# Performance work log

Measured on AMD Instinct MI355X. Metric: run time of the kernel, lower is better.

The kernel has to match this reference:

```python
import jax, jax.numpy as jnp
import numpy as np

N = 50000
E = 1600000
EPS = 1e-5


def setup_inputs() -> dict:
    key = jax.random.key(0)
    ks = jax.random.split(key, 10)
    x = jax.random.normal(ks[0], (N, 128), dtype=jnp.float32)
    edge_row = jax.random.randint(ks[1], (E,), 0, N, dtype=jnp.int32)
    edge_col = jax.random.randint(ks[2], (E,), 0, N, dtype=jnp.int32)
    edge_weight = jax.random.uniform(ks[3], (E,), dtype=jnp.float32)
    # kaiming-ish scaled weights
    W0 = jax.random.normal(ks[4], (128, 128), dtype=jnp.float32) / np.sqrt(128)
    b0 = jax.random.normal(ks[5], (128,), dtype=jnp.float32) * 0.01
    W1 = jax.random.normal(ks[6], (128, 128), dtype=jnp.float32) / np.sqrt(128)
    b1 = jax.random.normal(ks[7], (128,), dtype=jnp.float32) * 0.01
    W2 = jax.random.normal(ks[8], (128, 40), dtype=jnp.float32) / np.sqrt(128)
    b2 = jax.random.normal(ks[9], (40,), dtype=jnp.float32) * 0.01
    g0 = jnp.ones((128,), jnp.float32)
    be0 = jnp.zeros((128,), jnp.float32)
    g1 = jnp.ones((128,), jnp.float32)
    be1 = jnp.zeros((128,), jnp.float32)
    return dict(x=x, edge_row=edge_row, edge_col=edge_col, edge_weight=edge_weight,
                W0=W0, b0=b0, g0=g0, be0=be0, W1=W1, b1=b1, g1=g1, be1=be1, W2=W2, b2=b2)


def _spmm(edge_row, edge_col, edge_weight, h):
    # adj_t @ h : gather source rows, scale by edge weight, scatter-add to dst
    msg = h[edge_col] * edge_weight[:, None]           # [E, F]
    return jax.ops.segment_sum(msg, edge_row, num_segments=N)  # [N, F]


def _gcn_conv(x, W, b, edge_row, edge_col, edge_weight):
    h = x @ W                                          # dense GEMM [N, F_out]
    return _spmm(edge_row, edge_col, edge_weight, h) + b


def _batchnorm(x, gamma, beta):
    # training-mode BatchNorm1d over node dim (biased variance, as torch uses)
    mean = jnp.mean(x, axis=0)
    var = jnp.mean(jnp.square(x - mean), axis=0)
    return (x - mean) * jax.lax.rsqrt(var + EPS) * gamma + beta


def reference(x, edge_row, edge_col, edge_weight,
              W0, b0, g0, be0, W1, b1, g1, be1, W2, b2):
    # layer 0: conv -> BN -> ReLU (dropout = identity for deterministic reference)
    h = _gcn_conv(x, W0, b0, edge_row, edge_col, edge_weight)
    h = jax.nn.relu(_batchnorm(h, g0, be0))
    # layer 1
    h = _gcn_conv(h, W1, b1, edge_row, edge_col, edge_weight)
    h = jax.nn.relu(_batchnorm(h, g1, be1))
    # final conv (no BN/ReLU)
    return _gcn_conv(h, W2, b2, edge_row, edge_col, edge_weight)
```

## Files before the change

### kernel.cpp

```cpp
#include <hip/hip_runtime.h>
#include <hip/hip_fp16.h>


constexpr int   N_NODES   = 50000;
constexpr int   E_EDGES   = 1600000;
constexpr float BN_EPS    = 1e-5f;
constexpr int   K_BUCKETS = (N_NODES + 255) / 256;
constexpr int   BCAP      = 10240;
constexpr int   CHUNK     = 4096;
constexpr int   PART_BLK  = (E_EDGES + CHUNK - 1) / CHUNK;
constexpr int   CG_SHIFT  = 13;
constexpr int   CG_N      = 8;
constexpr int   AITER     = CHUNK / 256;
constexpr int   TEAMS40   = 6;

typedef _Float16 f16x8 __attribute__((ext_vector_type(8)));
typedef float    f32x4 __attribute__((ext_vector_type(4)));
typedef float    f32x2 __attribute__((ext_vector_type(2)));

__device__ __forceinline__ float dec_w(unsigned u) {
  return __half2float(__ushort_as_half((unsigned short)(u >> 16)));
}

__global__ __launch_bounds__(128) void prep_ker(const float* __restrict__ W0,
                                                const float* __restrict__ W1,
                                                const float* __restrict__ W2,
                                                __half* __restrict__ wt0,
                                                __half* __restrict__ wt1,
                                                __half* __restrict__ wt2,
                                                float* __restrict__ zstats) {
  const int b = blockIdx.x;
  const int k = threadIdx.x;
  if (b == 0) {
#pragma unroll
    for (int j = 0; j < 6; ++j) zstats[k * 6 + j] = 0.f;
  }
  if (b < 128) {
    wt0[b * 128 + k] = __float2half_rn(W0[k * 128 + b]);
  } else if (b < 256) {
    const int n = b - 128;
    wt1[n * 128 + k] = __float2half_rn(W1[k * 128 + n]);
  } else {
    const int n = b - 256;
    const float v = (n < 40) ? W2[k * 40 + n] : 0.f;
    wt2[n * 128 + k] = __float2half_rn(v);
  }
}

__global__ __launch_bounds__(256) void partA_ker(const int* __restrict__ rows,
                                                 const int* __restrict__ cols,
                                                 const float* __restrict__ ew,
                                                 int* __restrict__ gcursor,
                                                 int2* __restrict__ ebuf) {
  __shared__ int  cnt[256], cnt2[256], sc[256], offs[256], gbase[256];
  __shared__ int2 buf[CHUNK];
  const int tid = threadIdx.x;
  cnt[tid] = 0; cnt2[tid] = 0;
  __syncthreads();

  const int e0   = blockIdx.x * CHUNK;
  const int ecnt = min(CHUNK, E_EDGES - e0);

  int2 held[AITER];
#pragma unroll
  for (int j = 0; j < AITER; ++j) {
    const int i = tid + j * 256;
    if (i < ecnt) {
      const int   r = rows[e0 + i];
      const int   c = cols[e0 + i];
      const float w = ew[e0 + i];
      held[j].x = c | ((int)__half_as_ushort(__float2half_rn(w)) << 16);
      held[j].y = r;
      atomicAdd(&cnt[r >> 8], 1);
    }
  }
  __syncthreads();

  sc[tid] = cnt[tid];
  __syncthreads();
  for (int o = 1; o < 256; o <<= 1) {
    int u = (tid >= o) ? sc[tid - o] : 0;
    __syncthreads();
    sc[tid] += u;
    __syncthreads();
  }
  offs[tid] = sc[tid] - cnt[tid];
  if (tid < K_BUCKETS && cnt[tid] > 0)
    gbase[tid] = atomicAdd(&gcursor[tid], cnt[tid]);
  __syncthreads();

#pragma unroll
  for (int j = 0; j < AITER; ++j) {
    const int i = tid + j * 256;
    if (i < ecnt) {
      const int b = held[j].y >> 8;
      const int p = offs[b] + atomicAdd(&cnt2[b], 1);
      buf[p] = held[j];
    }
  }
  __syncthreads();

  for (int i = tid; i < ecnt; i += 256) {
    const int2 v   = buf[i];
    const int  b   = v.y >> 8;
    const int  idx = gbase[b] + (i - offs[b]);
    if (idx < BCAP) ebuf[(long)b * BCAP + idx] = v;
  }
}

__global__ __launch_bounds__(256) void partB_ker(const int* __restrict__ gcursor,
                                                 const int2* __restrict__ ebuf,
                                                 unsigned* __restrict__ se,
                                                 int* __restrict__ rowptr) {
  const int b   = blockIdx.x;
  const int tid = threadIdx.x;
  __shared__ int cnt[256 * CG_N], cur[256 * CG_N], sh[256];
  __shared__ int sbase;

  const int gv = (tid < K_BUCKETS) ? gcursor[tid] : 0;
  sh[tid] = gv;
  __syncthreads();
  for (int o = 1; o < 256; o <<= 1) {
    int u = (tid >= o) ? sh[tid - o] : 0;
    __syncthreads();
    sh[tid] += u;
    __syncthreads();
  }
  if (tid == b) sbase = sh[tid] - gv;
  if (b == 0 && tid == 0) rowptr[N_NODES] = E_EDGES;

#pragma unroll
  for (int j = 0; j < CG_N; ++j) {
    cnt[tid * CG_N + j] = 0;
    cur[tid * CG_N + j] = 0;
  }
  __syncthreads();
  const int base = sbase;
  const int cntb = min(gcursor[b], BCAP);

  const int2* __restrict__ src = ebuf + (long)b * BCAP;
  for (int i = tid; i < cntb; i += 256) {
    const int2 v = src[i];
    const int key = (v.y & 255) * CG_N + ((v.x & 0xFFFF) >> CG_SHIFT);
    atomicAdd(&cnt[key], 1);
  }
  __syncthreads();

  int loc[CG_N];
  int s = 0;
#pragma unroll
  for (int j = 0; j < CG_N; ++j) { loc[j] = s; s += cnt[tid * CG_N + j]; }
  sh[tid] = s;
  __syncthreads();
  for (int o = 1; o < 256; o <<= 1) {
    int u = (tid >= o) ? sh[tid - o] : 0;
    __syncthreads();
    sh[tid] += u;
    __syncthreads();
  }
  const int tb = sh[tid] - s;
#pragma unroll
  for (int j = 0; j < CG_N; ++j) cnt[tid * CG_N + j] = tb + loc[j];
  const int grow = b * 256 + tid;
  if (grow < N_NODES) rowptr[grow] = base + tb;
  __syncthreads();

  for (int i = tid; i < cntb; i += 256) {
    const int2 v   = src[i];
    const int  key = (v.y & 255) * CG_N + ((v.x & 0xFFFF) >> CG_SHIFT);
    const int  p   = cnt[key] + atomicAdd(&cur[key], 1);
    se[base + p] = (unsigned)v.x;
  }
}

template <int FOUT, int FOUT_PAD, bool FUSE, bool OUT_FP8, typename XT>
__global__ __launch_bounds__(256) void gemm_mfma_ker(const XT* __restrict__ X,
                                                     const __half* __restrict__ Wt,
                                                     void* __restrict__ Hout,
                                                     const float* __restrict__ stats,
                                                     const float* __restrict__ g,
                                                     const float* __restrict__ be) {
  constexpr int CT    = FOUT_PAD / 16;
  constexpr int PITCH = 136;

  __shared__ _Float16 Xs[64 * PITCH];
  __shared__ _Float16 Ws[FOUT_PAD * PITCH];
  __shared__ float ssc[128], ssh[128];

  const int tid  = threadIdx.x;
  const int row0 = blockIdx.x * 64;

  if constexpr (FUSE) {
    if (tid < 128) {
      const float mean = stats[tid] * (1.0f / N_NODES);
      const float var  = stats[128 + tid] * (1.0f / N_NODES) - mean * mean;
      const float sc   = g[tid] * rsqrtf(var + BN_EPS);
      ssc[tid] = sc;
      ssh[tid] = be[tid] - mean * sc;
    }
    __syncthreads();
  }

  for (int i = tid; i < FOUT_PAD * 16; i += 256) {
    const int r  = i >> 4;
    const int c8 = (i & 15) * 8;
    *(f16x8*)(Ws + r * PITCH + c8) = *(const f16x8*)(Wt + r * 128 + c8);
  }

  if constexpr (sizeof(XT) == 4) {
    for (int i = tid; i < 64 * 32; i += 256) {
      const int r  = i >> 5;
      const int k4 = (i & 31) * 4;
      const int gr = min(row0 + r, N_NODES - 1);
      float4 v = *(const float4*)((const float*)X + (long)gr * 128 + k4);
      _Float16* d = Xs + r * PITCH + k4;
      d[0] = (_Float16)v.x; d[1] = (_Float16)v.y;
      d[2] = (_Float16)v.z; d[3] = (_Float16)v.w;
    }
  } else {
    for (int i = tid; i < 64 * 16; i += 256) {
      const int r  = i >> 4;
      const int k8 = (i & 15) * 8;
      const int gr = min(row0 + r, N_NODES - 1);
      f16x8 v = *(const f16x8*)((const _Float16*)X + (long)gr * 128 + k8);
      if constexpr (FUSE) {
#pragma unroll
        for (int j = 0; j < 8; ++j)
          v[j] = (_Float16)fmaxf((float)v[j] * ssc[k8 + j] + ssh[k8 + j], 0.f);
      }
      *(f16x8*)(Xs + r * PITCH + k8) = v;
    }
  }
  __syncthreads();

  const int wave = tid >> 6;
  const int lane = tid & 63;
  const int m    = lane & 15;
  const int q    = lane >> 4;
  const int rw   = wave * 16;

  f16x8 af[4];
  {
    const _Float16* ab = Xs + (rw + m) * PITCH + q * 8;
#pragma unroll
    for (int ks = 0; ks < 4; ++ks) af[ks] = *(const f16x8*)(ab + ks * 32);
  }

  f32x4 acc[CT];
#pragma unroll
  for (int ct = 0; ct < CT; ++ct) acc[ct] = (f32x4){0.f, 0.f, 0.f, 0.f};

#pragma unroll
  for (int ct = 0; ct < CT; ++ct) {
    const _Float16* bb = Ws + (ct * 16 + m) * PITCH + q * 8;
#pragma unroll
    for (int ks = 0; ks < 4; ++ks) {
      const f16x8 bf = *(const f16x8*)(bb + ks * 32);
      acc[ct] = __builtin_amdgcn_mfma_f32_16x16x32_f16(af[ks], bf, acc[ct], 0, 0, 0);
    }
  }

  __syncthreads();
#pragma unroll
  for (int ct = 0; ct < CT; ++ct) {
#pragma unroll
    for (int reg = 0; reg < 4; ++reg) {
      Xs[(rw + q * 4 + reg) * PITCH + ct * 16 + m] = (_Float16)acc[ct][reg];
    }
  }
  __syncthreads();

  if constexpr (OUT_FP8) {
    constexpr int C16 = FOUT / 16;
    unsigned char* H8 = (unsigned char*)Hout;
    for (int i = tid; i < 64 * C16; i += 256) {
      const int r   = i / C16;
      const int c16 = (i % C16) * 16;
      const int gr  = row0 + r;
      if (gr < N_NODES) {
        const _Float16* src = Xs + r * PITCH + c16;
        int w[4];
#pragma unroll
        for (int j = 0; j < 4; ++j) {
          int p = __builtin_amdgcn_cvt_pk_fp8_f32((float)src[4 * j + 0],
                                                  (float)src[4 * j + 1], 0, false);
          p = __builtin_amdgcn_cvt_pk_fp8_f32((float)src[4 * j + 2],
                                              (float)src[4 * j + 3], p, true);
          w[j] = p;
        }
        *(int4*)(H8 + (long)gr * FOUT + c16) = make_int4(w[0], w[1], w[2], w[3]);
      }
    }
  } else {
    constexpr int C8 = FOUT / 8;
    __half* H16 = (__half*)Hout;
    for (int i = tid; i < 64 * C8; i += 256) {
      const int r  = i / C8;
      const int c8 = (i % C8) * 8;
      const int gr = row0 + r;
      if (gr < N_NODES)
        *(f16x8*)(H16 + (long)gr * FOUT + c8) = *(const f16x8*)(Xs + r * PITCH + c8);
    }
  }
}

__global__ __launch_bounds__(256) void spmm_fp8_ker(const int* __restrict__ rowptr,
                                                    const unsigned* __restrict__ se,
                                                    const unsigned char* __restrict__ H,
                                                    __half* __restrict__ A) {
  const int gid  = blockIdx.x * 256 + threadIdx.x;
  const int lane = threadIdx.x & 63;
  const int wid  = __builtin_amdgcn_readfirstlane(gid >> 6);
  if (wid >= N_NODES) return;
  const int beg = rowptr[wid];
  const int end = rowptr[wid + 1];
  const ushort* __restrict__ Hl = (const ushort*)H + lane;
  float acc0 = 0.f, acc1 = 0.f;

#define FP8_EDGE(U)                                                            \
  {                                                                            \
    const unsigned u_ = (U);                                                   \
    const f32x2 v_ = __builtin_amdgcn_cvt_pk_f32_fp8((int)Hl[(u_ & 0xFFFF) * 64], false); \
    const float w_ = dec_w(u_);                                                \
    acc0 += w_ * v_[0]; acc1 += w_ * v_[1];                                    \
  }

  int e = beg;
  for (; e < end && (e & 3); ++e) FP8_EDGE(se[e]);
  for (; e + 8 <= end; e += 8) {
    const uint4 a = *(const uint4*)(se + e);
    const uint4 b = *(const uint4*)(se + e + 4);
    FP8_EDGE(a.x) FP8_EDGE(a.y) FP8_EDGE(a.z) FP8_EDGE(a.w)
    FP8_EDGE(b.x) FP8_EDGE(b.y) FP8_EDGE(b.z) FP8_EDGE(b.w)
  }
  for (; e + 4 <= end; e += 4) {
    const uint4 a = *(const uint4*)(se + e);
    FP8_EDGE(a.x) FP8_EDGE(a.y) FP8_EDGE(a.z) FP8_EDGE(a.w)
  }
  for (; e < end; ++e) FP8_EDGE(se[e]);
#undef FP8_EDGE

  ((__half2*)A)[(long)wid * 64 + lane] = __floats2half2_rn(acc0, acc1);
}

__global__ __launch_bounds__(256) void spmm_csr40_ker(const int* __restrict__ rowptr,
                                                      const unsigned* __restrict__ se,
                                                      const __half* __restrict__ H,
                                                      const float* __restrict__ b,
                                                      float* __restrict__ out) {
  const int t    = threadIdx.x;
  const int team = t / 40;
  const int l    = t % 40;
  if (team >= TEAMS40) return;
  const int wid = blockIdx.x * TEAMS40 + team;
  if (wid >= N_NODES) return;
  const int beg = rowptr[wid];
  const int end = rowptr[wid + 1];
  float acc = 0.f;

#define F40_EDGE(U)                                                            \
  {                                                                            \
    const unsigned u_ = (U);                                                   \
    acc += dec_w(u_) * __half2float(H[(long)(u_ & 0xFFFF) * 40 + l]);          \
  }

  int e = beg;
  for (; e < end && (e & 3); ++e) F40_EDGE(se[e]);
  for (; e + 8 <= end; e += 8) {
    const uint4 a = *(const uint4*)(se + e);
    const uint4 c = *(const uint4*)(se + e + 4);
    F40_EDGE(a.x) F40_EDGE(a.y) F40_EDGE(a.z) F40_EDGE(a.w)
    F40_EDGE(c.x) F40_EDGE(c.y) F40_EDGE(c.z) F40_EDGE(c.w)
  }
  for (; e + 4 <= end; e += 4) {
    const uint4 a = *(const uint4*)(se + e);
    F40_EDGE(a.x) F40_EDGE(a.y) F40_EDGE(a.z) F40_EDGE(a.w)
  }
  for (; e < end; ++e) F40_EDGE(se[e]);
#undef F40_EDGE

  __builtin_nontemporal_store(acc + b[l], out + (long)wid * 40 + l);
}

constexpr int BN_BLOCKS   = 512;
constexpr int BN_ROWS_PER = (N_NODES + BN_BLOCKS - 1) / BN_BLOCKS;

__global__ __launch_bounds__(256) void bn_stats_ker(const __half* __restrict__ A,
                                                    float* __restrict__ stats) {
  __shared__ float s_sh[128], q_sh[128];
  const int tid = threadIdx.x;
  if (tid < 128) { s_sh[tid] = 0.f; q_sh[tid] = 0.f; }
  __syncthreads();

  const int c2 = (tid & 63) * 2;
  const int rs = tid >> 6;
  const int r0 = blockIdx.x * BN_ROWS_PER;
  const int re = min(r0 + BN_ROWS_PER, N_NODES);
  float s0 = 0.f, s1 = 0.f, q0 = 0.f, q1 = 0.f;
  for (int r = r0 + rs; r < re; r += 4) {
    const float2 v = __half22float2(*(const __half2*)(A + (long)r * 128 + c2));
    s0 += v.x; q0 += v.x * v.x;
    s1 += v.y; q1 += v.y * v.y;
  }
  atomicAdd(&s_sh[c2 + 0], s0);
  atomicAdd(&s_sh[c2 + 1], s1);
  atomicAdd(&q_sh[c2 + 0], q0);
  atomicAdd(&q_sh[c2 + 1], q1);
  __syncthreads();
  if (tid < 128) {
    atomicAdd(&stats[tid],       s_sh[tid]);
    atomicAdd(&stats[128 + tid], q_sh[tid]);
  }
}

extern "C" void kernel_launch(void* const* d_in, const int* in_sizes, int n_in,
                              void* d_out, int out_size, void* d_ws, size_t ws_size,
                              hipStream_t stream) {
  const float* x    = (const float*)d_in[0];
  const int*   erow = (const int*)d_in[1];
  const int*   ecol = (const int*)d_in[2];
  const float* ew   = (const float*)d_in[3];
  const float* W0   = (const float*)d_in[4];
  const float* g0   = (const float*)d_in[6];
  const float* be0  = (const float*)d_in[7];
  const float* W1   = (const float*)d_in[8];
  const float* g1   = (const float*)d_in[10];
  const float* be1  = (const float*)d_in[11];
  const float* W2   = (const float*)d_in[12];
  const float* b2   = (const float*)d_in[13];
  float* out = (float*)d_out;

  unsigned char* h  = (unsigned char*)d_ws;
  __half*   agg     = (__half*)(h + (long)N_NODES * 256);
  float*    stats0  = (float*)(agg + (long)N_NODES * 128);
  float*    stats1  = stats0 + 256;
  int*      gcursor = (int*)(stats1 + 256);
  int*      rowptr  = gcursor + 256;
  unsigned* se      = (unsigned*)(rowptr + 50004);
  int2*     ebuf    = (int2*)(se + E_EDGES);
  __half*   wt0     = (__half*)(ebuf + (long)K_BUCKETS * BCAP);
  __half*   wt1     = wt0 + 128 * 128;
  __half*   wt2     = wt1 + 128 * 128;

  const int g_gemm   = (N_NODES + 63) / 64;
  const int g_spmm   = (N_NODES * 64) / 256;
  const int g_spmm40 = (N_NODES + TEAMS40 - 1) / TEAMS40;

  prep_ker<<<304, 128, 0, stream>>>(W0, W1, W2, wt0, wt1, wt2, stats0);

  partA_ker<<<PART_BLK, 256, 0, stream>>>(erow, ecol, ew, gcursor, ebuf);
  partB_ker<<<K_BUCKETS, 256, 0, stream>>>(gcursor, ebuf, se, rowptr);

  gemm_mfma_ker<128, 128, false, true, float><<<g_gemm, 256, 0, stream>>>(
      x, wt0, h, nullptr, nullptr, nullptr);
  spmm_fp8_ker<<<g_spmm, 256, 0, stream>>>(rowptr, se, h, agg);
  bn_stats_ker<<<BN_BLOCKS, 256, 0, stream>>>(agg, stats0);

  gemm_mfma_ker<128, 128, true, true, _Float16><<<g_gemm, 256, 0, stream>>>(
      (const _Float16*)agg, wt1, h, stats0, g0, be0);
  spmm_fp8_ker<<<g_spmm, 256, 0, stream>>>(rowptr, se, h, agg);
  bn_stats_ker<<<BN_BLOCKS, 256, 0, stream>>>(agg, stats1);

  gemm_mfma_ker<40, 48, true, false, _Float16><<<g_gemm, 256, 0, stream>>>(
      (const _Float16*)agg, wt2, h, stats1, g1, be1);
  spmm_csr40_ker<<<g_spmm40, 256, 0, stream>>>(rowptr, se, (const __half*)h, b2, out);
}
```

Before: 315.1 us.

## Split FP8 SpMM wave into half-waves per edge pair and vectorize partition loads

The FP8 SpMM kernel now has each half-wave handle a different edge, with each lane loading 4 FP8 values (32-bit) instead of 2. The two halves' partial sums are combined with a cross-lane shuffle, which doubles the bytes per gather load and halves the number of dependent gather iterations per row. The partition kernel also reads rows, cols and weights with int4/float4 loads for full chunks, which changes which edges each thread holds. The cost is an extra shuffle reduction, more accumulator registers, a padded zero-weight edge for odd counts, and a strided per-thread access pattern in the partition load.

```diff
diff --git a/kernel.cpp b/kernel.cpp
--- a/kernel.cpp
+++ b/kernel.cpp
@@ -60,18 +60,40 @@
 
   const int e0   = blockIdx.x * CHUNK;
   const int ecnt = min(CHUNK, E_EDGES - e0);
+  const bool full = (ecnt == CHUNK);
 
   int2 held[AITER];
-#pragma unroll
-  for (int j = 0; j < AITER; ++j) {
-    const int i = tid + j * 256;
-    if (i < ecnt) {
-      const int   r = rows[e0 + i];
-      const int   c = cols[e0 + i];
-      const float w = ew[e0 + i];
-      held[j].x = c | ((int)__half_as_ushort(__float2half_rn(w)) << 16);
-      held[j].y = r;
-      atomicAdd(&cnt[r >> 8], 1);
+  if (full) {
+    const int4*   r4 = (const int4*)(rows + e0) + tid * (AITER / 4);
+    const int4*   c4 = (const int4*)(cols + e0) + tid * (AITER / 4);
+    const float4* w4 = (const float4*)(ew + e0) + tid * (AITER / 4);
+#pragma unroll
+    for (int v = 0; v < AITER / 4; ++v) {
+      const int4   r = r4[v];
+      const int4   c = c4[v];
+      const float4 w = w4[v];
+      const int rr[4] = {r.x, r.y, r.z, r.w};
+      const int cc[4] = {c.x, c.y, c.z, c.w};
+      const float ww[4] = {w.x, w.y, w.z, w.w};
+#pragma unroll
+      for (int s = 0; s < 4; ++s) {
+        held[v * 4 + s].x = cc[s] | ((int)__half_as_ushort(__float2half_rn(ww[s])) << 16);
+        held[v * 4 + s].y = rr[s];
+        atomicAdd(&cnt[rr[s] >> 8], 1);
+      }
+    }
+  } else {
+#pragma unroll
+    for (int j = 0; j < AITER; ++j) {
+      const int i = tid + j * 256;
+      if (i < ecnt) {
+        const int   r = rows[e0 + i];
+        const int   c = cols[e0 + i];
+        const float w = ew[e0 + i];
+        held[j].x = c | ((int)__half_as_ushort(__float2half_rn(w)) << 16);
+        held[j].y = r;
+        atomicAdd(&cnt[r >> 8], 1);
+      }
     }
   }
   __syncthreads();
@@ -91,8 +113,7 @@
 
 #pragma unroll
   for (int j = 0; j < AITER; ++j) {
-    const int i = tid + j * 256;
-    if (i < ecnt) {
+    if (full || (tid + j * 256) < ecnt) {
       const int b = held[j].y >> 8;
       const int p = offs[b] + atomicAdd(&cnt2[b], 1);
       buf[p] = held[j];
@@ -310,37 +331,68 @@
                                                     __half* __restrict__ A) {
   const int gid  = blockIdx.x * 256 + threadIdx.x;
   const int lane = threadIdx.x & 63;
+  const int hsel = lane >> 5;
+  const int l32  = lane & 31;
   const int wid  = __builtin_amdgcn_readfirstlane(gid >> 6);
   if (wid >= N_NODES) return;
   const int beg = rowptr[wid];
   const int end = rowptr[wid + 1];
-  const ushort* __restrict__ Hl = (const ushort*)H + lane;
-  float acc0 = 0.f, acc1 = 0.f;
-
-#define FP8_EDGE(U)                                                            \
-  {                                                                            \
-    const unsigned u_ = (U);                                                   \
-    const f32x2 v_ = __builtin_amdgcn_cvt_pk_f32_fp8((int)Hl[(u_ & 0xFFFF) * 64], false); \
-    const float w_ = dec_w(u_);                                                \
-    acc0 += w_ * v_[0]; acc1 += w_ * v_[1];                                    \
+  const unsigned* __restrict__ Hl = (const unsigned*)H + l32;
+  float a0 = 0.f, a1 = 0.f, a2 = 0.f, a3 = 0.f;
+
+#define PAIR(U0, U1)                                                            \
+  {                                                                             \
+    const unsigned u_  = hsel ? (U1) : (U0);                                    \
+    const unsigned d_  = Hl[(u_ & 0xFFFF) * 32];                                \
+    const float    w_  = dec_w(u_);                                             \
+    const f32x2    lo_ = __builtin_amdgcn_cvt_pk_f32_fp8((int)d_, false);       \
+    const f32x2    hi_ = __builtin_amdgcn_cvt_pk_f32_fp8((int)d_, true);        \
+    a0 += w_ * lo_[0]; a1 += w_ * lo_[1];                                       \
+    a2 += w_ * hi_[0]; a3 += w_ * hi_[1];                                       \
   }
 
   int e = beg;
-  for (; e < end && (e & 3); ++e) FP8_EDGE(se[e]);
-  for (; e + 8 <= end; e += 8) {
+  {
+    const int head = min(end - e, (4 - (e & 3)) & 3);
+    for (int i = 0; i < head; i += 2) {
+      const unsigned u0 = se[e + i];
+      const unsigned u1 = (i + 1 < head) ? se[e + i + 1] : 0u;
+      PAIR(u0, u1)
+    }
+    e += head;
+  }
+  for (; e + 16 <= end; e += 16) {
     const uint4 a = *(const uint4*)(se + e);
     const uint4 b = *(const uint4*)(se + e + 4);
-    FP8_EDGE(a.x) FP8_EDGE(a.y) FP8_EDGE(a.z) FP8_EDGE(a.w)
-    FP8_EDGE(b.x) FP8_EDGE(b.y) FP8_EDGE(b.z) FP8_EDGE(b.w)
+    const uint4 c = *(const uint4*)(se + e + 8);
+    const uint4 d = *(const uint4*)(se + e + 12);
+    PAIR(a.x, a.y) PAIR(a.z, a.w) PAIR(b.x, b.y) PAIR(b.z, b.w)
+    PAIR(c.x, c.y) PAIR(c.z, c.w) PAIR(d.x, d.y) PAIR(d.z, d.w)
   }
   for (; e + 4 <= end; e += 4) {
     const uint4 a = *(const uint4*)(se + e);
-    FP8_EDGE(a.x) FP8_EDGE(a.y) FP8_EDGE(a.z) FP8_EDGE(a.w)
-  }
-  for (; e < end; ++e) FP8_EDGE(se[e]);
-#undef FP8_EDGE
-
-  ((__half2*)A)[(long)wid * 64 + lane] = __floats2half2_rn(acc0, acc1);
+    PAIR(a.x, a.y) PAIR(a.z, a.w)
+  }
+  for (; e < end; e += 2) {
+    const unsigned u0 = se[e];
+    const unsigned u1 = (e + 1 < end) ? se[e + 1] : 0u;
+    PAIR(u0, u1)
+  }
+#undef PAIR
+
+  a0 += __shfl_xor(a0, 32, 64);
+  a1 += __shfl_xor(a1, 32, 64);
+  a2 += __shfl_xor(a2, 32, 64);
+  a3 += __shfl_xor(a3, 32, 64);
+
+  if (lane < 32) {
+    const __half2 h01 = __floats2half2_rn(a0, a1);
+    const __half2 h23 = __floats2half2_rn(a2, a3);
+    uint2 st;
+    st.x = *(const unsigned*)&h01;
+    st.y = *(const unsigned*)&h23;
+    *(uint2*)((__half*)A + (long)wid * 128 + l32 * 4) = st;
+  }
 }
 
 __global__ __launch_bounds__(256) void spmm_csr40_ker(const int* __restrict__ rowptr,
```

Result: faster. 306.7 us (-2.6%).
